# Kernel optimization log

Measured on AMD Instinct MI355X. Metric: run time of the kernel, lower is better.

The kernel has to match this reference:

```python
import jax, jax.numpy as jnp
import numpy as np

N_NODES = 100000
N_EDGES = 1600000
N_GRAPHS = 1024
EMB = 32
HID = 64
N_CLASSES = 10
N_SHAPE = 16
N_COLOR = 8


def setup_inputs() -> dict:
    key = jax.random.key(0)
    ks = jax.random.split(key, 12)
    shape_id = jax.random.randint(ks[0], (N_NODES,), 0, N_SHAPE + 1, dtype=jnp.int32)
    color_id = jax.random.randint(ks[1], (N_NODES,), 0, N_COLOR + 1, dtype=jnp.int32)
    edge_index = jax.random.randint(ks[2], (2, N_EDGES), 0, N_NODES, dtype=jnp.int32)
    batch = jnp.sort(jax.random.randint(ks[3], (N_NODES,), 0, N_GRAPHS, dtype=jnp.int32))
    shape_table = jax.random.normal(ks[4], (N_SHAPE + 1, EMB), jnp.float32)
    color_table = jax.random.normal(ks[5], (N_COLOR + 1, EMB), jnp.float32)
    W1 = jax.random.normal(ks[6], (EMB, HID), jnp.float32) / np.sqrt(EMB)
    b1 = jnp.zeros((HID,), jnp.float32)
    W2 = jax.random.normal(ks[7], (HID, HID), jnp.float32) / np.sqrt(HID)
    b2 = jnp.zeros((HID,), jnp.float32)
    Wl = jax.random.normal(ks[8], (HID, N_CLASSES), jnp.float32) / np.sqrt(HID)
    bl = jnp.zeros((N_CLASSES,), jnp.float32)
    return dict(shape_id=shape_id, color_id=color_id, edge_index=edge_index, batch=batch,
                shape_table=shape_table, color_table=color_table,
                W1=W1, b1=b1, W2=W2, b2=b2, Wl=Wl, bl=bl)


def gcn_conv(x, W, b, src, dst, num_nodes):
    # PyG GCNConv: add self-loops, symmetric normalization D^-1/2 (A+I) D^-1/2
    h = x @ W  # [N, out]
    deg = 1.0 + jax.ops.segment_sum(jnp.ones_like(dst, jnp.float32), dst, num_segments=num_nodes)
    dis = jax.lax.rsqrt(deg)  # deg >= 1 due to self-loop
    norm = dis[src] * dis[dst]  # [E]
    agg = jax.ops.segment_sum(h[src] * norm[:, None], dst, num_segments=num_nodes)
    agg = agg + h * (dis * dis)[:, None]  # self-loop term
    return agg + b


def reference(shape_id, color_id, edge_index, batch, shape_table, color_table,
              W1, b1, W2, b2, Wl, bl):
    # padding_idx=0 -> row 0 contributes zeros
    st = shape_table.at[0].set(0.0)
    ct = color_table.at[0].set(0.0)
    x = st[shape_id] + ct[color_id]  # [N, emb]
    src, dst = edge_index[0], edge_index[1]
    x = jax.nn.relu(gcn_conv(x, W1, b1, src, dst, N_NODES))
    x = jax.nn.relu(gcn_conv(x, W2, b2, src, dst, N_NODES))
    # global_mean_pool over batch ids
    sums = jax.ops.segment_sum(x, batch, num_segments=N_GRAPHS)
    cnts = jax.ops.segment_sum(jnp.ones((x.shape[0],), x.dtype), batch, num_segments=N_GRAPHS)
    pooled = sums / jnp.maximum(cnts, 1.0)[:, None]  # [B, hidden]
    return pooled @ Wl + bl  # [B, num_classes]
```

## Files before the change

### kernel.cpp

```cpp
#include <hip/hip_runtime.h>
#include <hip/hip_bf16.h>
#include <hip/hip_fp16.h>

#define N_NODES   100000
#define N_EDGES   1600000
#define N_GRAPHS  1024
#define EMB       32
#define HID       64
#define N_CLASSES 10
#define SCAN_BLOCKS 391
#define NCOMBO 153
#define BUCK_NODES 448
#define NBUCK 224
#define BIN_CAP 8192
#define EPB 4096

typedef _Float16 f16x8 __attribute__((ext_vector_type(8)));
typedef float f32x4 __attribute__((ext_vector_type(4)));

__global__ __launch_bounds__(256) void prep_kernel(
    const int* __restrict__ sid, const int* __restrict__ cid,
    const int* __restrict__ batch, int* __restrict__ combo, int* __restrict__ gstart,
    const float* __restrict__ st, const float* __restrict__ ct,
    const float* __restrict__ W1, __half* __restrict__ TCh,
    float* __restrict__ pooled, int* __restrict__ gcur) {
    int t = threadIdx.x;
    int v = blockIdx.x * 256 + t;
    if (v < N_GRAPHS * HID) pooled[v] = 0.0f;
    if (blockIdx.x == 0 && t < NBUCK) gcur[t] = 0;
    if (v < N_NODES) {
        combo[v] = sid[v] * 9 + cid[v];
        int b = batch[v];
        int bp = (v == 0) ? -1 : batch[v - 1];
        for (int g = bp + 1; g <= b; ++g) gstart[g] = v;
        if (v == N_NODES - 1) {
            for (int g = b + 1; g <= N_GRAPHS; ++g) gstart[g] = N_NODES;
        }
    }
    if (blockIdx.x < NCOMBO && t >= 64 && t < 128) {
        int r = blockIdx.x, j = t - 64;
        int s = r / 9, c = r % 9;
        float acc = 0.0f;
        if (s != 0) {
#pragma unroll
            for (int k = 0; k < EMB; ++k) acc = fmaf(st[s * EMB + k], W1[k * HID + j], acc);
        }
        if (c != 0) {
#pragma unroll
            for (int k = 0; k < EMB; ++k) acc = fmaf(ct[c * EMB + k], W1[k * HID + j], acc);
        }
        TCh[r * HID + j] = __float2half_rn(acc);
    }
}

__global__ __launch_bounds__(512) void binA_kernel(
    const int* __restrict__ src, const int* __restrict__ dst,
    const int* __restrict__ combo, int* __restrict__ gcur,
    int* __restrict__ gbinx, int* __restrict__ gbiny) {
    __shared__ int2 stg[EPB];
    __shared__ int hist[NBUCK];
    __shared__ int base[NBUCK + 1];
    __shared__ int gstart[NBUCK];
    __shared__ int scanbuf[256];
    int t = threadIdx.x;
    int e0 = blockIdx.x * EPB;
    for (int i = t; i < NBUCK; i += 512) hist[i] = 0;
    __syncthreads();

    int2 myq[8];
    int mybo[8];
#pragma unroll
    for (int i = 0; i < 8; ++i) {
        int e = e0 + t + i * 512;
        if (e < N_EDGES) {
            int d = dst[e];
            int s = src[e];
            unsigned b = (unsigned)d / BUCK_NODES;
            int off = atomicAdd(&hist[b], 1);
            myq[i].x = s | (combo[s] << 17);
            myq[i].y = d;
            mybo[i] = (int)(b << 16) | off;
        } else {
            mybo[i] = -1;
        }
    }
    __syncthreads();

    int h = (t < NBUCK) ? hist[t] : 0;
    if (t < 256) scanbuf[t] = h;
    __syncthreads();
#pragma unroll
    for (int off = 1; off < 256; off <<= 1) {
        int x = (t < 256 && t >= off) ? scanbuf[t - off] : 0;
        __syncthreads();
        if (t < 256) scanbuf[t] += x;
        __syncthreads();
    }
    if (t < NBUCK) base[t] = scanbuf[t] - h;
    if (t == 0) base[NBUCK] = scanbuf[255];
    __syncthreads();
#pragma unroll
    for (int i = 0; i < 8; ++i) {
        if (mybo[i] >= 0) {
            int b = mybo[i] >> 16, off = mybo[i] & 0xFFFF;
            stg[base[b] + off] = myq[i];
        }
    }
    if (t < NBUCK) {
        int n = hist[t];
        gstart[t] = n ? atomicAdd(&gcur[t], n) : 0;
    }
    __syncthreads();
    int total = base[NBUCK];
    for (int i = t; i < total; i += 512) {
        int2 q = stg[i];
        unsigned b = (unsigned)q.y / BUCK_NODES;
        size_t pos = (size_t)b * BIN_CAP + gstart[b] + (i - base[b]);
        gbinx[pos] = q.x;
        gbiny[pos] = q.y;
    }
}

__global__ __launch_bounds__(512) void bucket_kernel(
    const int* __restrict__ gbiny, const int* __restrict__ gcur,
    float* __restrict__ dis, int* __restrict__ rowptr) {
    __shared__ int ldeg[BUCK_NODES];
    __shared__ int s[512];
    __shared__ int sc[256];
    int b = blockIdx.x, t = threadIdx.x;
    if (t < 256) sc[t] = (t < NBUCK) ? gcur[t] : 0;
    for (int i = t; i < BUCK_NODES; i += 512) ldeg[i] = 0;
    __syncthreads();
#pragma unroll
    for (int off = 1; off < 256; off <<= 1) {
        int x = (t < 256 && t >= off) ? sc[t - off] : 0;
        __syncthreads();
        if (t < 256) sc[t] += x;
        __syncthreads();
    }
    int bb = (b == 0) ? 0 : sc[b - 1];
    int n = gcur[b];
    const int* mybin = gbiny + (size_t)b * BIN_CAP;
    for (int i = t; i < n; i += 512)
        atomicAdd(&ldeg[mybin[i] - b * BUCK_NODES], 1);
    __syncthreads();
    int d = (t < BUCK_NODES) ? ldeg[t] : 0;
    int v = b * BUCK_NODES + t;
    if (t < BUCK_NODES && v < N_NODES) dis[v] = rsqrtf(1.0f + (float)d);
    s[t] = d;
    __syncthreads();
#pragma unroll
    for (int off = 1; off < 512; off <<= 1) {
        int x = (t >= off) ? s[t - off] : 0;
        __syncthreads();
        s[t] += x;
        __syncthreads();
    }
    if (t < BUCK_NODES && v < N_NODES) rowptr[v] = bb + s[t] - d;
    if (b == 0 && t == 0) rowptr[N_NODES] = N_EDGES;
}

__global__ __launch_bounds__(1024) void binB_kernel(
    const int* __restrict__ gbinx, const int* __restrict__ gbiny,
    const int* __restrict__ gcur,
    const int* __restrict__ rowptr, const float* __restrict__ dis,
    int2* __restrict__ epack) {
    __shared__ int curs[BUCK_NODES];
    int b = blockIdx.x, t = threadIdx.x;
    for (int i = t; i < BUCK_NODES; i += 1024) curs[i] = 0;
    __syncthreads();
    int n = gcur[b];
    const int* mx = gbinx + (size_t)b * BIN_CAP;
    const int* my = gbiny + (size_t)b * BIN_CAP;
    for (int i = t; i < n; i += 1024) {
        int qx = mx[i];
        int qy = my[i];
        int local = qy - b * BUCK_NODES;
        int r = atomicAdd(&curs[local], 1);
        unsigned sx = (unsigned)qx;
        int srci = (int)(sx & 0x1FFFF);
        int comboOff = (int)((sx >> 17) * 128u);
        int2 rec;
        rec.x = (srci << 15) | comboOff;
        rec.y = __float_as_int(dis[srci]);
        epack[rowptr[qy] + r] = rec;
    }
}

#define AGG_CHUNK(Q, LBASE, J0)                                                \
    _Pragma("unroll")                                                          \
    for (int i = 0; i < 8; ++i) {                                              \
        int off = __builtin_amdgcn_readlane((Q).x, (LBASE) + i) & 0x7FFF;      \
        int wb  = __builtin_amdgcn_readlane((Q).y, (LBASE) + i);               \
        off = ((J0) + i < cnt) ? off : 0;                                      \
        wb  = ((J0) + i < cnt) ? wb  : 0;                                      \
        __half tv = *(const __half*)((const char*)TCs + (off + lane2));        \
        acc = fmaf(__int_as_float(wb), __half2float(tv), acc);                 \
    }

#define AGG_NODE(N, RS, RE, DV, CO)                                            \
    {                                                                          \
        int deg = (RE) - (RS);                                                 \
        int cnt = deg > 32 ? 32 : deg;                                         \
        float acc = 0.0f;                                                      \
        AGG_CHUNK(q1, (N)*16, 0)                                               \
        if (cnt > 8)  { AGG_CHUNK(q1, (N)*16 + 8, 8) }                         \
        if (cnt > 16) { AGG_CHUNK(q2, (N)*16, 16) }                            \
        if (cnt > 24) { AGG_CHUNK(q2, (N)*16 + 8, 24) }                        \
        if (deg > 32) {                                                        \
            for (int e = (RS) + 32; e < (RE); ++e) {                           \
                int2 q = epack[e];                                             \
                __half tv = *(const __half*)((const char*)TCs +                \
                                             ((q.x & 0x7FFF) + lane2));        \
                acc = fmaf(__int_as_float(q.y), __half2float(tv), acc);        \
            }                                                                  \
        }                                                                      \
        __half hv = *(const __half*)((const char*)TCs + ((CO) + lane2));       \
        float val = (DV) * fmaf(__half2float(hv), (DV), acc) + bias;           \
        val = val > 0.0f ? val : 0.0f;                                         \
        xsA[w * 4 + (N)][lane] = __float2half_rn(val * (DV));                  \
    }

__global__ __launch_bounds__(256, 6) void agg1_mm2_kernel(
    const int2* __restrict__ epack, const int* __restrict__ rowptr,
    const int* __restrict__ combo, const float* __restrict__ dis,
    const __half* __restrict__ TCh, const float* __restrict__ W2,
    const float* __restrict__ b1, __half* __restrict__ h2s) {
    __shared__ __align__(16) __half TCs[NCOMBO * HID];
    __shared__ __align__(16) __half xsA[16][72];
    __shared__ __align__(16) __half Dst[16 * 64];
    int t = threadIdx.x;
    int lane = t & 63, w = t >> 6;
    int lane2 = lane * 2;
    int vb = blockIdx.x * 16;
    int v0 = vb + w * 4;

    int sub = lane >> 4, sl = lane & 15;
    int rb = rowptr[v0 + sub];
    int2 q1 = epack[rb + sl];
    int2 q2 = epack[rb + 16 + sl];

    int r0 = __builtin_amdgcn_readfirstlane(rowptr[v0]);
    int r1 = __builtin_amdgcn_readfirstlane(rowptr[v0 + 1]);
    int r2 = __builtin_amdgcn_readfirstlane(rowptr[v0 + 2]);
    int r3 = __builtin_amdgcn_readfirstlane(rowptr[v0 + 3]);
    int r4 = __builtin_amdgcn_readfirstlane(rowptr[v0 + 4]);

    float d0 = dis[v0], d1 = dis[v0 + 1], d2 = dis[v0 + 2], d3 = dis[v0 + 3];
    int o0 = combo[v0] << 7, o1 = combo[v0 + 1] << 7;
    int o2 = combo[v0 + 2] << 7, o3 = combo[v0 + 3] << 7;
    float bias = b1[lane];

    f16x8 bf0, bf1;
    {
        int colw = (w << 4) + (lane & 15);
        int kb = (lane >> 4) * 8;
#pragma unroll
        for (int i = 0; i < 8; ++i) {
            bf0[i] = (_Float16)W2[(kb + i) * HID + colw];
            bf1[i] = (_Float16)W2[(32 + kb + i) * HID + colw];
        }
    }

    {
        const int4* s4 = (const int4*)TCh;
        int4* dd4 = (int4*)TCs;
        for (int i = t; i < NCOMBO * HID * 2 / 16; i += 256) dd4[i] = s4[i];
    }
    __syncthreads();

    AGG_NODE(0, r0, r1, d0, o0)
    AGG_NODE(1, r1, r2, d1, o1)
    AGG_NODE(2, r2, r3, d2, o2)
    AGG_NODE(3, r3, r4, d3, o3)

    __syncthreads();

    const __half* xa = &xsA[lane & 15][0];
    f16x8 a0 = *(const f16x8*)(xa + (lane >> 4) * 8);
    f16x8 a1 = *(const f16x8*)(xa + 32 + (lane >> 4) * 8);
    f32x4 dacc = {0.0f, 0.0f, 0.0f, 0.0f};
    dacc = __builtin_amdgcn_mfma_f32_16x16x32_f16(a0, bf0, dacc, 0, 0, 0);
    dacc = __builtin_amdgcn_mfma_f32_16x16x32_f16(a1, bf1, dacc, 0, 0, 0);

    {
        int colg = (w << 4) + (lane & 15);
#pragma unroll
        for (int i = 0; i < 4; ++i)
            Dst[((lane >> 4) * 4 + i) * 64 + colg] = __float2half_rn(dacc[i]);
    }
    __syncthreads();

    {
        const uint2* ds2 = (const uint2*)Dst;
        uint2* go = (uint2*)(h2s + (size_t)vb * HID);
        go[t] = ds2[t];
    }
}

__device__ __forceinline__ float agg2_node(const int* __restrict__ epackx, int sx,
                                           int rs, int re, int lane, int lane2,
                                           const __half* __restrict__ h2s) {
    float acc = 0.0f;
    int p = rs;
    for (;;) {
        int avail = re - p;
        int cnt = avail > 64 ? 64 : avail;
        int vo = (int)((((unsigned)sx) >> 15) << 7);
        int j = 0;
        for (; j + 8 <= cnt; j += 8) {
            float g[8];
#pragma unroll
            for (int i = 0; i < 8; ++i) {
                int off = __builtin_amdgcn_readlane(vo, j + i);
                g[i] = __half2float(*(const __half*)((const char*)h2s + (off + lane2)));
            }
#pragma unroll
            for (int i = 0; i < 8; ++i) acc += g[i];
        }
        if (j < cnt) {
#pragma unroll
            for (int i = 0; i < 8; ++i) {
                int jj = j + i;
                int off = __builtin_amdgcn_readlane(vo, jj & 63);
                float gv = __half2float(*(const __half*)((const char*)h2s + (off + lane2)));
                acc += (jj < cnt) ? gv : 0.0f;
            }
        }
        p += 64;
        if (p >= re) break;
        int idx = p + lane;
        idx = idx < N_EDGES ? idx : N_EDGES - 1;
        sx = epackx[idx * 2];
    }
    return acc;
}

__global__ __launch_bounds__(256, 8) void agg2_pool_kernel(
    const int2* __restrict__ epack, const int* __restrict__ rowptr,
    const __half* __restrict__ h2s, const float* __restrict__ dis,
    const float* __restrict__ b2, const int* __restrict__ batch,
    float* __restrict__ pooled) {
    int t = threadIdx.x, lane = t & 63, w = t >> 6;
    int lane2 = lane * 2;
    const int* epackx = (const int*)epack;
    int v0 = (blockIdx.x * 4 + w) * 4;

    int r0 = __builtin_amdgcn_readfirstlane(rowptr[v0]);
    int r1 = __builtin_amdgcn_readfirstlane(rowptr[v0 + 1]);
    int r2 = __builtin_amdgcn_readfirstlane(rowptr[v0 + 2]);
    int r3 = __builtin_amdgcn_readfirstlane(rowptr[v0 + 3]);
    int r4 = __builtin_amdgcn_readfirstlane(rowptr[v0 + 4]);

    int ia = r0 + lane; ia = ia < N_EDGES ? ia : N_EDGES - 1;
    int ib = r1 + lane; ib = ib < N_EDGES ? ib : N_EDGES - 1;
    int ic = r2 + lane; ic = ic < N_EDGES ? ic : N_EDGES - 1;
    int id = r3 + lane; id = id < N_EDGES ? id : N_EDGES - 1;
    int sa = epackx[ia * 2];
    int sb = epackx[ib * 2];
    int sc = epackx[ic * 2];
    int sd = epackx[id * 2];

    float bv = b2[lane];
    float acc0 = agg2_node(epackx, sa, r0, r1, lane, lane2, h2s);
    float acc1 = agg2_node(epackx, sb, r1, r2, lane, lane2, h2s);
    float acc2 = agg2_node(epackx, sc, r2, r3, lane, lane2, h2s);
    float acc3 = agg2_node(epackx, sd, r3, r4, lane, lane2, h2s);

#define AGG2_VAL(V, ACC, OUT)                                                  \
    {                                                                          \
        float dv = dis[V];                                                     \
        float self = __half2float(h2s[(size_t)(V) * HID + lane]);              \
        float val = dv * ((ACC) + self) + bv;                                  \
        OUT = val > 0.0f ? val : 0.0f;                                         \
    }
    float val0, val1, val2, val3;
    AGG2_VAL(v0, acc0, val0)
    AGG2_VAL(v0 + 1, acc1, val1)
    AGG2_VAL(v0 + 2, acc2, val2)
    AGG2_VAL(v0 + 3, acc3, val3)
#undef AGG2_VAL

    int g0 = __builtin_amdgcn_readfirstlane(batch[v0]);
    int g1 = __builtin_amdgcn_readfirstlane(batch[v0 + 1]);
    int g2 = __builtin_amdgcn_readfirstlane(batch[v0 + 2]);
    int g3 = __builtin_amdgcn_readfirstlane(batch[v0 + 3]);
    float s = val0; int g = g0;
    if (g1 == g) { s += val1; } else { unsafeAtomicAdd(&pooled[g * HID + lane], s); g = g1; s = val1; }
    if (g2 == g) { s += val2; } else { unsafeAtomicAdd(&pooled[g * HID + lane], s); g = g2; s = val2; }
    if (g3 == g) { s += val3; } else { unsafeAtomicAdd(&pooled[g * HID + lane], s); g = g3; s = val3; }
    unsafeAtomicAdd(&pooled[g * HID + lane], s);
}

__global__ __launch_bounds__(64) void logits_kernel(
    const float* __restrict__ pooled, const int* __restrict__ gstart,
    const float* __restrict__ Wl, const float* __restrict__ bl,
    float* __restrict__ out) {
    __shared__ float row[HID];
    int g = blockIdx.x, t = threadIdx.x;
    int c = gstart[g + 1] - gstart[g]; if (c < 1) c = 1;
    row[t] = pooled[g * HID + t] / (float)c;
    __syncthreads();
    if (t < N_CLASSES) {
        float acc = bl[t];
#pragma unroll
        for (int k = 0; k < HID; ++k) acc = fmaf(row[k], Wl[k * N_CLASSES + t], acc);
        out[g * N_CLASSES + t] = acc;
    }
}

extern "C" void kernel_launch(void* const* d_in, const int* in_sizes, int n_in,
                              void* d_out, int out_size, void* d_ws, size_t ws_size,
                              hipStream_t stream) {
    const int*   shape_id = (const int*)d_in[0];
    const int*   color_id = (const int*)d_in[1];
    const int*   edge_idx = (const int*)d_in[2];
    const int*   batch    = (const int*)d_in[3];
    const float* st       = (const float*)d_in[4];
    const float* ct       = (const float*)d_in[5];
    const float* W1       = (const float*)d_in[6];
    const float* b1       = (const float*)d_in[7];
    const float* W2       = (const float*)d_in[8];
    const float* b2       = (const float*)d_in[9];
    const float* Wl       = (const float*)d_in[10];
    const float* bl       = (const float*)d_in[11];
    float* out = (float*)d_out;

    const int* src = edge_idx;
    const int* dst = edge_idx + N_EDGES;

    char* ws = (char*)d_ws;
    int*    combo   = (int*)   (ws + 0);
    float*  dis     = (float*) (ws + 400384);
    int*    gstart  = (int*)   (ws + 801792);
    int*    rowptr  = (int*)   (ws + 1201152);
    __half* TCh     = (__half*)(ws + 1603584);
    float*  pooled  = (float*) (ws + 1623552);
    int*    gcur    = (int*)   (ws + 1889792);
    int2*   epack   = (int2*)  (ws + 1890816);
    int*    gbinx   = (int*)   (ws + 14690816);
    int*    gbiny   = (int*)   (ws + 22030848);
    __half* h2s     = (__half*)(ws + 29370880);

    prep_kernel<<<SCAN_BLOCKS, 256, 0, stream>>>(shape_id, color_id, batch, combo, gstart,
                                                 st, ct, W1, TCh, pooled, gcur);

    binA_kernel<<<(N_EDGES + EPB - 1) / EPB, 512, 0, stream>>>(src, dst, combo, gcur,
                                                               gbinx, gbiny);

    bucket_kernel<<<NBUCK, 512, 0, stream>>>(gbiny, gcur, dis, rowptr);

    binB_kernel<<<NBUCK, 1024, 0, stream>>>(gbinx, gbiny, gcur, rowptr, dis, epack);

    agg1_mm2_kernel<<<6250, 256, 0, stream>>>(epack, rowptr, combo, dis, TCh, W2, b1, h2s);

    agg2_pool_kernel<<<6250, 256, 0, stream>>>(epack, rowptr, h2s, dis, b2, batch, pooled);

    logits_kernel<<<N_GRAPHS, 64, 0, stream>>>(pooled, gstart, Wl, bl, out);
}
```

Measured before the change: 196.7 us.

## Fuse bucket and scatter kernels, shrink edge records to one int

Merges the degree/rowptr bucket kernel with the CSR scatter kernel into a single 1024-thread block per bucket. The dst ids are cached in shared memory and rowptr bases are kept locally, which removes one launch and one global re-read of the bins. Edge records drop from int2 to int, so the source dis weight is no longer stored. The agg1 kernel now gathers dis[src] on the fly, adding an indirect load per edge in exchange for halving the edge-array traffic. agg2 reads a contiguous int array instead of a stride-2 access.

```diff
diff --git a/kernel.cpp b/kernel.cpp
--- a/kernel.cpp
+++ b/kernel.cpp
@@ -121,15 +121,18 @@
     }
 }
 
-__global__ __launch_bounds__(512) void bucket_kernel(
-    const int* __restrict__ gbiny, const int* __restrict__ gcur,
-    float* __restrict__ dis, int* __restrict__ rowptr) {
+__global__ __launch_bounds__(1024) void bucket_scatter_kernel(
+    const int* __restrict__ gbinx, const int* __restrict__ gbiny,
+    const int* __restrict__ gcur,
+    float* __restrict__ dis, int* __restrict__ rowptr, int* __restrict__ epack4) {
+    __shared__ int ybin[BIN_CAP];
     __shared__ int ldeg[BUCK_NODES];
+    __shared__ int rbase[BUCK_NODES];
     __shared__ int s[512];
     __shared__ int sc[256];
     int b = blockIdx.x, t = threadIdx.x;
     if (t < 256) sc[t] = (t < NBUCK) ? gcur[t] : 0;
-    for (int i = t; i < BUCK_NODES; i += 512) ldeg[i] = 0;
+    for (int i = t; i < BUCK_NODES; i += 1024) ldeg[i] = 0;
     __syncthreads();
 #pragma unroll
     for (int off = 1; off < 256; off <<= 1) {
@@ -140,58 +143,54 @@
     }
     int bb = (b == 0) ? 0 : sc[b - 1];
     int n = gcur[b];
-    const int* mybin = gbiny + (size_t)b * BIN_CAP;
-    for (int i = t; i < n; i += 512)
-        atomicAdd(&ldeg[mybin[i] - b * BUCK_NODES], 1);
+    {
+        const int* my = gbiny + (size_t)b * BIN_CAP;
+        for (int i = t; i < n; i += 1024) {
+            int y = my[i];
+            ybin[i] = y;
+            atomicAdd(&ldeg[y - b * BUCK_NODES], 1);
+        }
+    }
     __syncthreads();
     int d = (t < BUCK_NODES) ? ldeg[t] : 0;
     int v = b * BUCK_NODES + t;
     if (t < BUCK_NODES && v < N_NODES) dis[v] = rsqrtf(1.0f + (float)d);
-    s[t] = d;
+    if (t < 512) s[t] = d;
     __syncthreads();
 #pragma unroll
     for (int off = 1; off < 512; off <<= 1) {
-        int x = (t >= off) ? s[t - off] : 0;
-        __syncthreads();
-        s[t] += x;
-        __syncthreads();
-    }
-    if (t < BUCK_NODES && v < N_NODES) rowptr[v] = bb + s[t] - d;
+        int x = (t < 512 && t >= off) ? s[t - off] : 0;
+        __syncthreads();
+        if (t < 512) s[t] += x;
+        __syncthreads();
+    }
+    if (t < BUCK_NODES) {
+        int rp = bb + s[t] - d;
+        rbase[t] = rp;
+        if (v < N_NODES) rowptr[v] = rp;
+    }
     if (b == 0 && t == 0) rowptr[N_NODES] = N_EDGES;
-}
-
-__global__ __launch_bounds__(1024) void binB_kernel(
-    const int* __restrict__ gbinx, const int* __restrict__ gbiny,
-    const int* __restrict__ gcur,
-    const int* __restrict__ rowptr, const float* __restrict__ dis,
-    int2* __restrict__ epack) {
-    __shared__ int curs[BUCK_NODES];
-    int b = blockIdx.x, t = threadIdx.x;
-    for (int i = t; i < BUCK_NODES; i += 1024) curs[i] = 0;
-    __syncthreads();
-    int n = gcur[b];
-    const int* mx = gbinx + (size_t)b * BIN_CAP;
-    const int* my = gbiny + (size_t)b * BIN_CAP;
-    for (int i = t; i < n; i += 1024) {
-        int qx = mx[i];
-        int qy = my[i];
-        int local = qy - b * BUCK_NODES;
-        int r = atomicAdd(&curs[local], 1);
-        unsigned sx = (unsigned)qx;
-        int srci = (int)(sx & 0x1FFFF);
-        int comboOff = (int)((sx >> 17) * 128u);
-        int2 rec;
-        rec.x = (srci << 15) | comboOff;
-        rec.y = __float_as_int(dis[srci]);
-        epack[rowptr[qy] + r] = rec;
-    }
-}
-
-#define AGG_CHUNK(Q, LBASE, J0)                                                \
+    for (int i = t; i < BUCK_NODES; i += 1024) ldeg[i] = 0;
+    __syncthreads();
+    {
+        const int* mx = gbinx + (size_t)b * BIN_CAP;
+        for (int i = t; i < n; i += 1024) {
+            int qx = mx[i];
+            int local = ybin[i] - b * BUCK_NODES;
+            int r = atomicAdd(&ldeg[local], 1);
+            unsigned sx = (unsigned)qx;
+            int srci = (int)(sx & 0x1FFFF);
+            int comboOff = (int)((sx >> 17) * 128u);
+            epack4[rbase[local] + r] = (srci << 15) | comboOff;
+        }
+    }
+}
+
+#define AGG_CHUNK(QX, DQ, LBASE, J0)                                           \
     _Pragma("unroll")                                                          \
     for (int i = 0; i < 8; ++i) {                                              \
-        int off = __builtin_amdgcn_readlane((Q).x, (LBASE) + i) & 0x7FFF;      \
-        int wb  = __builtin_amdgcn_readlane((Q).y, (LBASE) + i);               \
+        int off = __builtin_amdgcn_readlane((QX), (LBASE) + i) & 0x7FFF;       \
+        int wb  = __builtin_amdgcn_readlane(__float_as_int(DQ), (LBASE) + i);  \
         off = ((J0) + i < cnt) ? off : 0;                                      \
         wb  = ((J0) + i < cnt) ? wb  : 0;                                      \
         __half tv = *(const __half*)((const char*)TCs + (off + lane2));        \
@@ -203,16 +202,17 @@
         int deg = (RE) - (RS);                                                 \
         int cnt = deg > 32 ? 32 : deg;                                         \
         float acc = 0.0f;                                                      \
-        AGG_CHUNK(q1, (N)*16, 0)                                               \
-        if (cnt > 8)  { AGG_CHUNK(q1, (N)*16 + 8, 8) }                         \
-        if (cnt > 16) { AGG_CHUNK(q2, (N)*16, 16) }                            \
-        if (cnt > 24) { AGG_CHUNK(q2, (N)*16 + 8, 24) }                        \
+        AGG_CHUNK(q1x, dq1, (N)*16, 0)                                         \
+        if (cnt > 8)  { AGG_CHUNK(q1x, dq1, (N)*16 + 8, 8) }                   \
+        if (cnt > 16) { AGG_CHUNK(q2x, dq2, (N)*16, 16) }                      \
+        if (cnt > 24) { AGG_CHUNK(q2x, dq2, (N)*16 + 8, 24) }                  \
         if (deg > 32) {                                                        \
             for (int e = (RS) + 32; e < (RE); ++e) {                           \
-                int2 q = epack[e];                                             \
+                int qx = epack4[e];                                            \
+                float dw = dis[(unsigned)qx >> 15];                            \
                 __half tv = *(const __half*)((const char*)TCs +                \
-                                             ((q.x & 0x7FFF) + lane2));        \
-                acc = fmaf(__int_as_float(q.y), __half2float(tv), acc);        \
+                                             ((qx & 0x7FFF) + lane2));         \
+                acc = fmaf(dw, __half2float(tv), acc);                         \
             }                                                                  \
         }                                                                      \
         __half hv = *(const __half*)((const char*)TCs + ((CO) + lane2));       \
@@ -222,7 +222,7 @@
     }
 
 __global__ __launch_bounds__(256, 6) void agg1_mm2_kernel(
-    const int2* __restrict__ epack, const int* __restrict__ rowptr,
+    const int* __restrict__ epack4, const int* __restrict__ rowptr,
     const int* __restrict__ combo, const float* __restrict__ dis,
     const __half* __restrict__ TCh, const float* __restrict__ W2,
     const float* __restrict__ b1, __half* __restrict__ h2s) {
@@ -237,8 +237,10 @@
 
     int sub = lane >> 4, sl = lane & 15;
     int rb = rowptr[v0 + sub];
-    int2 q1 = epack[rb + sl];
-    int2 q2 = epack[rb + 16 + sl];
+    int q1x = epack4[rb + sl];
+    int q2x = epack4[rb + 16 + sl];
+    float dq1 = dis[(unsigned)q1x >> 15];
+    float dq2 = dis[(unsigned)q2x >> 15];
 
     int r0 = __builtin_amdgcn_readfirstlane(rowptr[v0]);
     int r1 = __builtin_amdgcn_readfirstlane(rowptr[v0 + 1]);
@@ -298,7 +300,7 @@
     }
 }
 
-__device__ __forceinline__ float agg2_node(const int* __restrict__ epackx, int sx,
+__device__ __forceinline__ float agg2_node(const int* __restrict__ epack4, int sx,
                                            int rs, int re, int lane, int lane2,
                                            const __half* __restrict__ h2s) {
     float acc = 0.0f;
@@ -331,19 +333,18 @@
         if (p >= re) break;
         int idx = p + lane;
         idx = idx < N_EDGES ? idx : N_EDGES - 1;
-        sx = epackx[idx * 2];
+        sx = epack4[idx];
     }
     return acc;
 }
 
 __global__ __launch_bounds__(256, 8) void agg2_pool_kernel(
-    const int2* __restrict__ epack, const int* __restrict__ rowptr,
+    const int* __restrict__ epack4, const int* __restrict__ rowptr,
     const __half* __restrict__ h2s, const float* __restrict__ dis,
     const float* __restrict__ b2, const int* __restrict__ batch,
     float* __restrict__ pooled) {
     int t = threadIdx.x, lane = t & 63, w = t >> 6;
     int lane2 = lane * 2;
-    const int* epackx = (const int*)epack;
     int v0 = (blockIdx.x * 4 + w) * 4;
 
     int r0 = __builtin_amdgcn_readfirstlane(rowptr[v0]);
@@ -356,16 +357,16 @@
     int ib = r1 + lane; ib = ib < N_EDGES ? ib : N_EDGES - 1;
     int ic = r2 + lane; ic = ic < N_EDGES ? ic : N_EDGES - 1;
     int id = r3 + lane; id = id < N_EDGES ? id : N_EDGES - 1;
-    int sa = epackx[ia * 2];
-    int sb = epackx[ib * 2];
-    int sc = epackx[ic * 2];
-    int sd = epackx[id * 2];
+    int sa = epack4[ia];
+    int sb = epack4[ib];
+    int sc = epack4[ic];
+    int sd = epack4[id];
 
     float bv = b2[lane];
-    float acc0 = agg2_node(epackx, sa, r0, r1, lane, lane2, h2s);
-    float acc1 = agg2_node(epackx, sb, r1, r2, lane, lane2, h2s);
-    float acc2 = agg2_node(epackx, sc, r2, r3, lane, lane2, h2s);
-    float acc3 = agg2_node(epackx, sd, r3, r4, lane, lane2, h2s);
+    float acc0 = agg2_node(epack4, sa, r0, r1, lane, lane2, h2s);
+    float acc1 = agg2_node(epack4, sb, r1, r2, lane, lane2, h2s);
+    float acc2 = agg2_node(epack4, sc, r2, r3, lane, lane2, h2s);
+    float acc3 = agg2_node(epack4, sd, r3, r4, lane, lane2, h2s);
 
 #define AGG2_VAL(V, ACC, OUT)                                                  \
     {                                                                          \
@@ -437,7 +438,7 @@
     __half* TCh     = (__half*)(ws + 1603584);
     float*  pooled  = (float*) (ws + 1623552);
     int*    gcur    = (int*)   (ws + 1889792);
-    int2*   epack   = (int2*)  (ws + 1890816);
+    int*    epack4  = (int*)   (ws + 1890816);
     int*    gbinx   = (int*)   (ws + 14690816);
     int*    gbiny   = (int*)   (ws + 22030848);
     __half* h2s     = (__half*)(ws + 29370880);
@@ -448,13 +449,12 @@
     binA_kernel<<<(N_EDGES + EPB - 1) / EPB, 512, 0, stream>>>(src, dst, combo, gcur,
                                                                gbinx, gbiny);
 
-    bucket_kernel<<<NBUCK, 512, 0, stream>>>(gbiny, gcur, dis, rowptr);
-
-    binB_kernel<<<NBUCK, 1024, 0, stream>>>(gbinx, gbiny, gcur, rowptr, dis, epack);
-
-    agg1_mm2_kernel<<<6250, 256, 0, stream>>>(epack, rowptr, combo, dis, TCh, W2, b1, h2s);
-
-    agg2_pool_kernel<<<6250, 256, 0, stream>>>(epack, rowptr, h2s, dis, b2, batch, pooled);
+    bucket_scatter_kernel<<<NBUCK, 1024, 0, stream>>>(gbinx, gbiny, gcur,
+                                                      dis, rowptr, epack4);
+
+    agg1_mm2_kernel<<<6250, 256, 0, stream>>>(epack4, rowptr, combo, dis, TCh, W2, b1, h2s);
+
+    agg2_pool_kernel<<<6250, 256, 0, stream>>>(epack4, rowptr, h2s, dis, b2, batch, pooled);
 
     logits_kernel<<<N_GRAPHS, 64, 0, stream>>>(pooled, gstart, Wl, bl, out);
 }
```

New measurement: 190.4 us. 1.03x faster.
